# Performance work log

Hardware: AMD Instinct MI355X
Metric: run time of the kernel (lower is better)

The kernel has to match this reference:

```python
import jax, jax.numpy as jnp
from jax import lax
import numpy as np

P1, P2, M1, M2, WIN, STEP = 7, 7, 18, 55, 37, 4


def _unfold(x, p):
    # x: [N,C,Hp,Wp] -> [N, C*p*p, Ho*Wo], torch.nn.functional.unfold ordering (C, di, dj)
    N, C, Hp, Wp = x.shape
    Ho, Wo = Hp - p + 1, Wp - p + 1
    cols = jnp.stack([x[:, :, i:i + Ho, j:j + Wo] for i in range(p) for j in range(p)], axis=2)
    return cols.reshape(N, C * p * p, Ho * Wo)


def _reflect_unfold(x, r, p):
    return _unfold(jnp.pad(x, ((0, 0), (0, 0), (r, r), (r, r)), mode='reflect'), p)


def _fold(X, p, oh, ow):
    # inverse of unfold (sum of overlapping patches), torch.nn.functional.fold
    N, n, L = X.shape
    Ho, Wo = oh - p + 1, ow - p + 1
    C = n // (p * p)
    Xr = X.reshape(N, C, p, p, Ho, Wo)
    out = jnp.zeros((N, C, oh, ow), X.dtype)
    for i in range(p):
        for j in range(p):
            out = out.at[:, :, i:i + Ho, j:j + Wo].add(Xr[:, :, i, j])
    return out


def _block_matching(x, m, p, w, s):
    # x: [N,1,H,W] -> flat patch indices [N, B*m] into the (H+w-1)x(W+w-1) unfold grid
    N, C, H, Wd = x.shape
    inc = w // 2
    xs = _reflect_unfold(x, p // 2 + inc, p).reshape(N, p * p, H + 2 * inc, Wd + 2 * inc)
    xc = xs[:, :, inc:inc + H:s, inc:inc + Wd:s]  # [N, p*p, Hs, Ws]
    Hs, Ws = xc.shape[2], xc.shape[3]
    offs = jnp.stack(jnp.meshgrid(jnp.arange(w), jnp.arange(w), indexing='ij'), axis=-1).reshape(-1, 2)
    def d_of(off):
        xo = lax.dynamic_slice(xs, (0, 0, off[0], off[1]), (N, p * p, H, Wd))[:, :, ::s, ::s]
        return jnp.sum((xo - xc) ** 2, axis=1)  # [N, Hs, Ws]
    dist = jnp.moveaxis(lax.map(d_of, offs), 0, 1)  # [N, w*w, Hs, Ws]
    dist = dist.at[:, inc * w + inc].set(-1.0)  # force self-match first
    _, idx = lax.top_k(-jnp.transpose(dist, (0, 2, 3, 1)), m)  # smallest m, sorted
    idx = jnp.transpose(idx, (0, 3, 1, 2))  # [N, m, Hs, Ws]
    ir = idx // w - inc
    ic = idx % w - inc
    rows = inc + s * jnp.arange(Hs)
    cols = inc + s * jnp.arange(Ws)
    flat = (ir + rows[None, None, :, None]) * (Wd + w - 1) + (ic + cols[None, None, None, :])
    return jnp.transpose(flat.reshape(N, m, Hs * Ws), (0, 2, 1)).reshape(N, -1)  # [N, B*m]


def _group_patches(unf, idx, m, n):
    # unf: [N, n, L], idx: [N, B*m] -> [N, B, m, n]
    N = unf.shape[0]
    g = jnp.take_along_axis(unf, idx[:, None, :], axis=2)  # [N, n, B*m]
    return jnp.transpose(g, (0, 2, 1)).reshape(N, -1, m, n)


def _denoise1(Y, sigma):
    m, n = Y.shape[2], Y.shape[3]
    YtY = jnp.einsum('abik,abjk->abij', Y, Y)
    rhs = YtY - (n * sigma ** 2) * jnp.eye(m, dtype=Y.dtype)
    theta = jnp.swapaxes(jnp.linalg.solve(YtY, rhs), -1, -2)
    Xh = theta @ Y
    wts = 1.0 / jnp.sum(theta ** 2, axis=3, keepdims=True)
    return Xh, wts


def _denoise2(Y, X, sigma):
    m, n = X.shape[2], X.shape[3]
    XtX = jnp.einsum('abik,abjk->abij', X, X)
    A = XtX + (n * sigma ** 2) * jnp.eye(m, dtype=X.dtype)
    theta = jnp.swapaxes(jnp.linalg.solve(A, XtX), -1, -2)
    Xh = theta @ Y
    wts = 1.0 / jnp.sum(theta ** 2, axis=3, keepdims=True)
    return Xh, wts


def _aggregation(Y, wts, idx, H, Wd, L, p, w):
    # Y: [N,B,m,n], wts: [N,B,m,1], idx: [N,B*m]; scatter-add into unfold grid, fold, normalize
    N, B, m, n = Y.shape
    Yw = jnp.transpose(Y * wts, (0, 3, 1, 2)).reshape(N, n, B * m)
    wflat = jnp.broadcast_to(wts.reshape(N, 1, B * m), (N, n, B * m))
    def scat(vals, ib):
        return jnp.zeros((n, L), vals.dtype).at[:, ib].add(vals)
    Xsum = jax.vmap(scat)(Yw, idx)
    div = jax.vmap(scat)(wflat, idx)
    oh, ow = H + w - 1 + p - 1, Wd + w - 1 + p - 1
    num = _fold(Xsum, p, oh, ow)
    den = _fold(div, p, oh, ow)
    r = w // 2 + p // 2
    return (num / den)[:, :, r:-r, r:-r]


def _nlridge(input_y, sigma):
    N, C, H, Wd = input_y.shape
    w, s = WIN, STEP
    # ---- step 1 ----
    p, m = P1, M1
    yb = jnp.mean(input_y, axis=1, keepdims=True)
    idx1 = _block_matching(lax.stop_gradient(yb), m, p, w, s)
    unf_y1 = _reflect_unfold(input_y, p // 2 + w // 2, p)
    Y1 = _group_patches(unf_y1, idx1, m, C * p * p)
    Xh1, w1 = _denoise1(Y1, sigma)
    den1 = _aggregation(Xh1, w1, idx1, H, Wd, unf_y1.shape[2], p, w)
    # ---- step 2 ----
    p, m = P2, M2
    xb = jnp.mean(den1, axis=1, keepdims=True)
    idx2 = _block_matching(lax.stop_gradient(xb), m, p, w, s)
    unf_y2 = _reflect_unfold(input_y, p // 2 + w // 2, p)
    unf_x2 = _reflect_unfold(den1, p // 2 + w // 2, p)
    Y2 = _group_patches(unf_y2, idx2, m, C * p * p)
    X2 = _group_patches(unf_x2, idx2, m, C * p * p)
    Xh2, w2 = _denoise2(Y2, X2, sigma)
    return _aggregation(Xh2, w2, idx2, H, Wd, unf_y2.shape[2], p, w)


def setup_inputs() -> dict:
    key = jax.random.key(0)
    k1 = jax.random.fold_in(key, 1)
    input_y = jax.random.uniform(k1, (1, 1, 256, 256), dtype=jnp.float32)
    sigma = jnp.asarray(0.1, dtype=jnp.float32)  # ~25/255 AWGN
    return {"input_y": input_y, "sigma": sigma}


def reference(input_y, sigma):
    return _nlridge(input_y, sigma)
```

## Files before the change

### kernel.cpp

```cpp
#include <hip/hip_runtime.h>
#include <math.h>
#include <float.h>

constexpr int IMG  = 256;
constexpr int PADR = 21;
constexpr int PDIM = IMG + 2*PADR;
constexpr int XDIM = PDIM - 7 + 1;
constexpr int LTOT = XDIM * XDIM;
constexpr int WSZ  = 37;
constexpr int INC  = 18;
constexpr int ST   = 4;
constexpr int GDIM = 64;
constexpr int NBLK = GDIM * GDIM;
constexpr int PS   = 7;
constexpr int PP   = 49;
constexpr int MM1  = 18;
constexpr int MM2  = 55;
constexpr int RG   = 43;
constexpr int NOFF = WSZ * WSZ;
constexpr int UCAP = (NOFF + 63) / 64;
constexpr int TDIM = 43;
constexpr int TSZ  = TDIM * TDIM;
constexpr int SLABSTRIDE = 2 * TSZ;

__global__ void pad_reflect(const float* __restrict__ src, float* __restrict__ dst)
{
    int idx = blockIdx.x * 256 + threadIdx.x;
    if (idx >= PDIM * PDIM) return;
    int y = idx / PDIM, x = idx % PDIM;
    int oy = y - PADR; oy = (oy < 0) ? -oy : ((oy >= IMG) ? 2*(IMG-1) - oy : oy);
    int ox = x - PADR; ox = (ox < 0) ? -ox : ((ox >= IMG) ? 2*(IMG-1) - ox : ox);
    dst[idx] = src[oy * IMG + ox];
}

__global__ __launch_bounds__(256) void block_match(const float* __restrict__ pad,
                                                   int* __restrict__ pos, int m)
{
    __shared__ float reg[RG][RG + 1];
    __shared__ float dist[NOFF];

    const int gi = blockIdx.y, gj = blockIdx.x;
    const int tid = threadIdx.x;
    const int r0 = ST * gi, c0 = ST * gj;

    for (int t = tid; t < RG * RG; t += 256) {
        int r = t / RG, c = t % RG;
        reg[r][c] = pad[(r0 + r) * PDIM + (c0 + c)];
    }
    __syncthreads();

    float q[PP];
#pragma unroll
    for (int i = 0; i < PS; i++)
#pragma unroll
        for (int j = 0; j < PS; j++)
            q[i * PS + j] = reg[INC + i][INC + j];

    for (int o = tid; o < NOFF; o += 256) {
        int oi = o / WSZ, oj = o % WSZ;
        float s = 0.f;
#pragma unroll
        for (int i = 0; i < PS; i++)
#pragma unroll
            for (int j = 0; j < PS; j++) {
                float d = reg[oi + i][oj + j] - q[i * PS + j];
                s += d * d;
            }
        dist[o] = (o == INC * WSZ + INC) ? -1.0f : s;
    }
    __syncthreads();

    if (tid >= 64) return;
    const int lane = tid;

    float dv[UCAP];
#pragma unroll
    for (int u = 0; u < UCAP; u++) {
        int o = lane + (u << 6);
        dv[u] = (o < NOFF) ? dist[o] : FLT_MAX;
    }

    const int blk = gi * GDIM + gj;
    for (int sel = 0; sel < m; sel++) {
        float bv = dv[0]; int bo = lane;
#pragma unroll
        for (int u = 1; u < UCAP; u++) {
            int o = lane + (u << 6);
            if (dv[u] < bv) { bv = dv[u]; bo = o; }
        }
#pragma unroll
        for (int d = 1; d < 64; d <<= 1) {
            float ov = __shfl_xor(bv, d);
            int   oo = __shfl_xor(bo, d);
            if (ov < bv || (ov == bv && oo < bo)) { bv = ov; bo = oo; }
        }
        if (lane == 0) {
            int oi = bo / WSZ, oj = bo % WSZ;
            pos[blk * m + sel] = (oi + ST * gi) * XDIM + (oj + ST * gj);
        }
#pragma unroll
        for (int u = 0; u < UCAP; u++)
            if (bo == lane + (u << 6)) dv[u] = FLT_MAX;
    }
}

template<int M_, bool ADDC, bool SLAB>
__global__ __launch_bounds__(256) void denoise_scatter(
    const float* __restrict__ padY, const float* __restrict__ padS,
    const int* __restrict__ pos, const float* __restrict__ sigma_p,
    float* __restrict__ dst, float* __restrict__ Wacc)
{
    constexpr int MP = (M_ + 4) & ~3;
    constexpr int SS = 52;
    constexpr int YS = 60;
    constexpr int UN = (2 * TSZ > M_ * SS) ? 2 * TSZ : M_ * SS;

    __shared__ __align__(16) float Yt [PP * YS];
    __shared__ __align__(16) float Msh[M_ * MP];
    __shared__ __align__(16) float SorT[UN];
    __shared__ float pcol[M_];
    __shared__ float wsh[M_];
    __shared__ int   posh[M_];

    float* Ssh  = SorT;
    float* tile = SorT;

    const int tid = threadIdx.x;
    const int blk = blockIdx.x;
    const float sg = *sigma_p;
    const float c  = (float)PP * sg * sg;

    if (tid < M_) posh[tid] = pos[blk * M_ + tid];
    __syncthreads();

    for (int t = tid; t < M_ * SS; t += 256) {
        int k = t / SS, qq = t - (t / SS) * SS;
        float v = 0.f;
        if (qq < PP) {
            int p_ = posh[k];
            int a = p_ / XDIM, b = p_ - (p_ / XDIM) * XDIM;
            v = padS[(a + qq / PS) * PDIM + (b + qq % PS)];
        }
        Ssh[t] = v;
    }
    __syncthreads();

    for (int t = tid; t < M_ * M_; t += 256) {
        int i = t / M_, j = t - (t / M_) * M_;
        if (j > i) continue;
        const float4* Si = (const float4*)&Ssh[i * SS];
        const float4* Sj = (const float4*)&Ssh[j * SS];
        float acc = 0.f;
#pragma unroll
        for (int cch = 0; cch < SS / 4; cch++) {
            float4 a4 = Si[cch], b4 = Sj[cch];
            acc += a4.x * b4.x + a4.y * b4.y + a4.z * b4.z + a4.w * b4.w;
        }
        if (ADDC && i == j) acc += c;
        Msh[i * MP + j] = acc;
    }
    __syncthreads();

    if (tid < 64) {
        const int j = (tid < M_) ? tid : (M_ - 1);
        float col[M_];
#pragma unroll
        for (int i = 0; i < M_; i++)
            col[i] = Msh[(i >= j) ? (i * MP + j) : (j * MP + i)];

#pragma unroll 1
        for (int k = 0; k < M_; k++) {
            if (tid == k) {
#pragma unroll
                for (int i = 0; i < M_; i++) pcol[i] = col[i];
            }
            float piv = pcol[j];
            float d   = pcol[k];
            d = (fabsf(d) > 1e-30f) ? d : 1e-30f;
            float dinv = 1.0f / d;
            bool  isk  = (j == k);
            float f    = isk ? (1.0f - dinv) : (piv * dinv);
            float fix  = isk ? (-dinv)       : (piv * dinv);
            float negf = -f;
#pragma unroll
            for (int i = 0; i < M_; i++) {
                float b   = __int_as_float(
                    __builtin_amdgcn_readlane(__float_as_int(col[i]), k));
                float upd = fmaf(b, negf, col[i]);
                col[i] = (i == k) ? fix : upd;
            }
        }
        if (tid < M_) {
            float s = 0.f;
#pragma unroll
            for (int i = 0; i < M_; i++) {
                float th = fmaf(c, col[i], (i == j) ? 1.f : 0.f);
                s = fmaf(th, th, s);
            }
            wsh[j] = 1.0f / s;
#pragma unroll
            for (int i = 0; i < M_; i++)
                Msh[i * MP + j] = -col[i];
        } else if (tid < MP) {
#pragma unroll
            for (int i = 0; i < M_; i++)
                Msh[i * MP + tid] = 0.f;
        }
    } else {
        const int t0 = tid - 64;
        for (int t = t0; t < PP * MP; t += 192) {
            int qq = t / MP, k = t - (t / MP) * MP;
            float v = 0.f;
            if (k < M_) {
                int p_ = posh[k];
                int a = p_ / XDIM, b = p_ - (p_ / XDIM) * XDIM;
                v = padY[(a + qq / PS) * PDIM + (b + qq % PS)];
            }
            Yt[qq * YS + k] = v;
        }
        if (SLAB)
            for (int t = t0; t < 2 * TSZ; t += 192) tile[t] = 0.f;
    }
    __syncthreads();

    constexpr int KP = (M_ + 1) / 2;
    constexpr int QP = (PP + 1) / 2;
    const int r0 = ST * (blk >> 6), c0 = ST * (blk & (GDIM - 1));
    for (int t = tid; t < KP * QP; t += 256) {
        int kp = t / QP, qp = t - (t / QP) * QP;
        int k0 = kp * 2, k1 = k0 + 1;
        int qq0 = qp * 2, qq1 = qq0 + 1;
        bool k1v = (k1 < M_), q1v = (qq1 < PP);
        int k1c  = k1v ? k1 : k0;
        int qq1c = q1v ? qq1 : qq0;
        const float4* G0 = (const float4*)&Msh[k0  * MP];
        const float4* G1 = (const float4*)&Msh[k1c * MP];
        const float4* Y0 = (const float4*)&Yt [qq0  * YS];
        const float4* Y1 = (const float4*)&Yt [qq1c * YS];
        float z00 = 0.f, z01 = 0.f, z10 = 0.f, z11 = 0.f;
#pragma unroll
        for (int cch = 0; cch < MP / 4; cch++) {
            float4 g0 = G0[cch], g1 = G1[cch], y0 = Y0[cch], y1 = Y1[cch];
            z00 += g0.x*y0.x + g0.y*y0.y + g0.z*y0.z + g0.w*y0.w;
            z01 += g0.x*y1.x + g0.y*y1.y + g0.z*y1.z + g0.w*y1.w;
            z10 += g1.x*y0.x + g1.y*y0.y + g1.z*y0.z + g1.w*y0.w;
            z11 += g1.x*y1.x + g1.y*y1.y + g1.z*y1.z + g1.w*y1.w;
        }
        float w0 = wsh[k0], w1 = k1v ? wsh[k1] : 0.f;
        int p0 = posh[k0], p1 = posh[k1c];
        float xh00 = (Yt[qq0  * YS + k0 ] - c * z00) * w0;
        float xh01 = (Yt[qq1c * YS + k0 ] - c * z01) * w0;
        float xh10 = (Yt[qq0  * YS + k1c] - c * z10) * w1;
        float xh11 = (Yt[qq1c * YS + k1c] - c * z11) * w1;
        int a0 = p0 / XDIM, b0 = p0 - (p0 / XDIM) * XDIM;
        int a1 = p1 / XDIM, b1 = p1 - (p1 / XDIM) * XDIM;
        int i0 = qq0 / PS, j0 = qq0 - i0 * PS;
        int i1 = qq1 / PS, j1 = qq1 - i1 * PS;
        if (SLAB) {
            int u0 = a0 - r0, v0 = b0 - c0, u1 = a1 - r0, v1 = b1 - c0;
            int l00 = (u0 + i0) * TDIM + v0 + j0;
            int l10 = (u1 + i0) * TDIM + v1 + j0;
            atomicAdd(&tile[l00], xh00); atomicAdd(&tile[TSZ + l00], w0);
            atomicAdd(&tile[l10], xh10); atomicAdd(&tile[TSZ + l10], w1);
            if (q1v) {
                int l01 = (u0 + i1) * TDIM + v0 + j1;
                int l11 = (u1 + i1) * TDIM + v1 + j1;
                atomicAdd(&tile[l01], xh01); atomicAdd(&tile[TSZ + l01], w0);
                atomicAdd(&tile[l11], xh11); atomicAdd(&tile[TSZ + l11], w1);
            }
        } else {
            atomicAdd(&dst[qq0 * LTOT + p0], xh00);
            if (q1v) atomicAdd(&dst[qq1 * LTOT + p0], xh01);
            if (k1v) {
                atomicAdd(&dst[qq0 * LTOT + p1], xh10);
                if (q1v) atomicAdd(&dst[qq1 * LTOT + p1], xh11);
            }
        }
    }
    if (SLAB) {
        __syncthreads();
        float* g = dst + (size_t)blk * SLABSTRIDE;
        for (int t = tid; t < 2 * TSZ; t += 256) g[t] = tile[t];
    } else {
        for (int t = tid; t < M_; t += 256)
            atomicAdd(&Wacc[posh[t]], wsh[t]);
    }
}

__global__ void fold_slab(const float* __restrict__ slab, float* __restrict__ out)
{
    int idx = blockIdx.x * 256 + threadIdx.x;
    if (idx >= IMG * IMG) return;
    int y = (idx >> 8) + PADR, x = (idx & 255) + PADR;
    int qy = y >> 2, ry = y & 3;
    int qx = x >> 2, rx = x & 3;
    float num = 0.f, den = 0.f;
    for (int di = 0; di < 11; di++) {
        int gi = qy - di;
        int li = 4 * di + ry;
        if ((unsigned)gi > (unsigned)(GDIM - 1) || li >= TDIM) continue;
        for (int dj = 0; dj < 11; dj++) {
            int gj = qx - dj;
            int lj = 4 * dj + rx;
            if ((unsigned)gj > (unsigned)(GDIM - 1) || lj >= TDIM) continue;
            const float* s = slab + (size_t)((gi << 6) + gj) * SLABSTRIDE + li * TDIM + lj;
            num += s[0];
            den += s[TSZ];
        }
    }
    out[idx] = num / den;
}

__global__ void fold_norm(const float* __restrict__ Xsum, const float* __restrict__ Wacc,
                          float* __restrict__ out)
{
    int idx = blockIdx.x * 256 + threadIdx.x;
    if (idx >= IMG * IMG) return;
    int y0 = idx / IMG, x0 = idx % IMG;
    int y = y0 + PADR, x = x0 + PADR;
    float num = 0.f, den = 0.f;
#pragma unroll
    for (int i = 0; i < PS; i++)
#pragma unroll
        for (int j = 0; j < PS; j++) {
            int a = y - i, b = x - j;
            num += Xsum[(i * PS + j) * LTOT + a * XDIM + b];
            den += Wacc[a * XDIM + b];
        }
    out[idx] = num / den;
}

extern "C" void kernel_launch(void* const* d_in, const int* in_sizes, int n_in,
                              void* d_out, int out_size, void* d_ws, size_t ws_size,
                              hipStream_t stream)
{
    const float* input = (const float*)d_in[0];
    const float* sigma = (const float*)d_in[1];
    float* out = (float*)d_out;

    char* ws = (char*)d_ws;
    float* padY = (float*)ws; ws += (size_t)PDIM * PDIM * 4;
    float* padX = (float*)ws; ws += (size_t)PDIM * PDIM * 4;
    float* den1 = (float*)ws; ws += (size_t)IMG * IMG * 4;
    int*   pos  = (int*)ws;   ws += (size_t)NBLK * MM2 * 4;
    size_t head = (size_t)(ws - (char*)d_ws);
    size_t slabBytes = (size_t)NBLK * SLABSTRIDE * 4;

    const int padBlocks = (PDIM * PDIM + 255) / 256;
    const int imgBlocks = (IMG * IMG + 255) / 256;

    if (ws_size >= head + slabBytes) {
        float* slab = (float*)ws;

        pad_reflect<<<padBlocks, 256, 0, stream>>>(input, padY);
        block_match<<<dim3(GDIM, GDIM), 256, 0, stream>>>(padY, pos, MM1);
        denoise_scatter<MM1, false, true><<<NBLK, 256, 0, stream>>>(padY, padY, pos, sigma,
                                                                    slab, nullptr);
        fold_slab<<<imgBlocks, 256, 0, stream>>>(slab, den1);

        pad_reflect<<<padBlocks, 256, 0, stream>>>(den1, padX);
        block_match<<<dim3(GDIM, GDIM), 256, 0, stream>>>(padX, pos, MM2);
        denoise_scatter<MM2, true, true><<<NBLK, 256, 0, stream>>>(padY, padX, pos, sigma,
                                                                   slab, nullptr);
        fold_slab<<<imgBlocks, 256, 0, stream>>>(slab, out);
    } else {
        float* Xsum = (float*)ws; ws += (size_t)PP * LTOT * 4;
        float* Wacc = (float*)ws;

        hipMemsetAsync(Xsum, 0, (size_t)PP * LTOT * 4, stream);
        hipMemsetAsync(Wacc, 0, (size_t)LTOT * 4, stream);
        pad_reflect<<<padBlocks, 256, 0, stream>>>(input, padY);
        block_match<<<dim3(GDIM, GDIM), 256, 0, stream>>>(padY, pos, MM1);
        denoise_scatter<MM1, false, false><<<NBLK, 256, 0, stream>>>(padY, padY, pos, sigma,
                                                                     Xsum, Wacc);
        fold_norm<<<imgBlocks, 256, 0, stream>>>(Xsum, Wacc, den1);

        pad_reflect<<<padBlocks, 256, 0, stream>>>(den1, padX);
        hipMemsetAsync(Xsum, 0, (size_t)PP * LTOT * 4, stream);
        hipMemsetAsync(Wacc, 0, (size_t)LTOT * 4, stream);
        block_match<<<dim3(GDIM, GDIM), 256, 0, stream>>>(padX, pos, MM2);
        denoise_scatter<MM2, true, false><<<NBLK, 256, 0, stream>>>(padY, padX, pos, sigma,
                                                                    Xsum, Wacc);
        fold_norm<<<imgBlocks, 256, 0, stream>>>(Xsum, Wacc, out);
    }
}
```

Measured before the change: 1.096 ms.

## Accumulate denoised patches directly into global slab to shrink LDS and raise occupancy

Removes the per-block shared-memory tile and performs the patch/weight atomic adds straight into the block's global slab, which is now zeroed with a memset before each step. Ssh and Yt share one LDS buffer, the Gram loop only enumerates lower-triangle entries via a sqrt index map, launch bounds request more waves per SIMD, and the k/q pairing changes from adjacent to half-split. This is meant to cut LDS footprint and raise occupancy. In exchange it trades fast LDS atomics for global atomics and adds two large memsets.

```diff
diff --git a/kernel.cpp b/kernel.cpp
--- a/kernel.cpp
+++ b/kernel.cpp
@@ -105,25 +105,25 @@
 }
 
 template<int M_, bool ADDC, bool SLAB>
-__global__ __launch_bounds__(256) void denoise_scatter(
+__global__ __launch_bounds__(256, 5) void denoise_scatter(
     const float* __restrict__ padY, const float* __restrict__ padS,
     const int* __restrict__ pos, const float* __restrict__ sigma_p,
     float* __restrict__ dst, float* __restrict__ Wacc)
 {
-    constexpr int MP = (M_ + 4) & ~3;
-    constexpr int SS = 52;
-    constexpr int YS = 60;
-    constexpr int UN = (2 * TSZ > M_ * SS) ? 2 * TSZ : M_ * SS;
-
-    __shared__ __align__(16) float Yt [PP * YS];
+    constexpr int MP  = (M_ + 4) & ~3;
+    constexpr int SS  = 52;
+    constexpr int YS  = 60;
+    constexpr int TRI = M_ * (M_ + 1) / 2;
+    constexpr int UNF = (M_ * SS > PP * YS) ? M_ * SS : PP * YS;
+
+    __shared__ __align__(16) float SY [UNF];
     __shared__ __align__(16) float Msh[M_ * MP];
-    __shared__ __align__(16) float SorT[UN];
     __shared__ float pcol[M_];
     __shared__ float wsh[M_];
     __shared__ int   posh[M_];
 
-    float* Ssh  = SorT;
-    float* tile = SorT;
+    float* Ssh = SY;
+    float* Yt  = SY;
 
     const int tid = threadIdx.x;
     const int blk = blockIdx.x;
@@ -145,9 +145,11 @@
     }
     __syncthreads();
 
-    for (int t = tid; t < M_ * M_; t += 256) {
-        int i = t / M_, j = t - (t / M_) * M_;
-        if (j > i) continue;
+    for (int t = tid; t < TRI; t += 256) {
+        int i = (int)((sqrtf((float)(8 * t + 1)) - 1.f) * 0.5f);
+        if ((i + 1) * (i + 2) / 2 <= t) i++;
+        else if (i * (i + 1) / 2 > t) i--;
+        int j = t - i * (i + 1) / 2;
         const float4* Si = (const float4*)&Ssh[i * SS];
         const float4* Sj = (const float4*)&Ssh[j * SS];
         float acc = 0.f;
@@ -218,18 +220,17 @@
             }
             Yt[qq * YS + k] = v;
         }
-        if (SLAB)
-            for (int t = t0; t < 2 * TSZ; t += 192) tile[t] = 0.f;
     }
     __syncthreads();
 
     constexpr int KP = (M_ + 1) / 2;
     constexpr int QP = (PP + 1) / 2;
     const int r0 = ST * (blk >> 6), c0 = ST * (blk & (GDIM - 1));
+    float* slab = SLAB ? (dst + (size_t)blk * SLABSTRIDE) : dst;
     for (int t = tid; t < KP * QP; t += 256) {
         int kp = t / QP, qp = t - (t / QP) * QP;
-        int k0 = kp * 2, k1 = k0 + 1;
-        int qq0 = qp * 2, qq1 = qq0 + 1;
+        int k0 = kp,  k1 = kp + KP;
+        int qq0 = qp, qq1 = qp + QP;
         bool k1v = (k1 < M_), q1v = (qq1 < PP);
         int k1c  = k1v ? k1 : k0;
         int qq1c = q1v ? qq1 : qq0;
@@ -254,34 +255,30 @@
         float xh11 = (Yt[qq1c * YS + k1c] - c * z11) * w1;
         int a0 = p0 / XDIM, b0 = p0 - (p0 / XDIM) * XDIM;
         int a1 = p1 / XDIM, b1 = p1 - (p1 / XDIM) * XDIM;
-        int i0 = qq0 / PS, j0 = qq0 - i0 * PS;
-        int i1 = qq1 / PS, j1 = qq1 - i1 * PS;
+        int i0 = qq0 / PS,  j0 = qq0 - i0 * PS;
+        int i1 = qq1c / PS, j1 = qq1c - i1 * PS;
         if (SLAB) {
             int u0 = a0 - r0, v0 = b0 - c0, u1 = a1 - r0, v1 = b1 - c0;
             int l00 = (u0 + i0) * TDIM + v0 + j0;
             int l10 = (u1 + i0) * TDIM + v1 + j0;
-            atomicAdd(&tile[l00], xh00); atomicAdd(&tile[TSZ + l00], w0);
-            atomicAdd(&tile[l10], xh10); atomicAdd(&tile[TSZ + l10], w1);
+            atomicAdd(&slab[l00], xh00); atomicAdd(&slab[TSZ + l00], w0);
+            if (k1v) { atomicAdd(&slab[l10], xh10); atomicAdd(&slab[TSZ + l10], w1); }
             if (q1v) {
                 int l01 = (u0 + i1) * TDIM + v0 + j1;
                 int l11 = (u1 + i1) * TDIM + v1 + j1;
-                atomicAdd(&tile[l01], xh01); atomicAdd(&tile[TSZ + l01], w0);
-                atomicAdd(&tile[l11], xh11); atomicAdd(&tile[TSZ + l11], w1);
+                atomicAdd(&slab[l01], xh01); atomicAdd(&slab[TSZ + l01], w0);
+                if (k1v) { atomicAdd(&slab[l11], xh11); atomicAdd(&slab[TSZ + l11], w1); }
             }
         } else {
-            atomicAdd(&dst[qq0 * LTOT + p0], xh00);
-            if (q1v) atomicAdd(&dst[qq1 * LTOT + p0], xh01);
+            atomicAdd(&slab[qq0 * LTOT + p0], xh00);
+            if (q1v) atomicAdd(&slab[qq1 * LTOT + p0], xh01);
             if (k1v) {
-                atomicAdd(&dst[qq0 * LTOT + p1], xh10);
-                if (q1v) atomicAdd(&dst[qq1 * LTOT + p1], xh11);
-            }
-        }
-    }
-    if (SLAB) {
-        __syncthreads();
-        float* g = dst + (size_t)blk * SLABSTRIDE;
-        for (int t = tid; t < 2 * TSZ; t += 256) g[t] = tile[t];
-    } else {
+                atomicAdd(&slab[qq0 * LTOT + p1], xh10);
+                if (q1v) atomicAdd(&slab[qq1 * LTOT + p1], xh11);
+            }
+        }
+    }
+    if (!SLAB) {
         for (int t = tid; t < M_; t += 256)
             atomicAdd(&Wacc[posh[t]], wsh[t]);
     }
@@ -352,12 +349,14 @@
     if (ws_size >= head + slabBytes) {
         float* slab = (float*)ws;
 
+        hipMemsetAsync(slab, 0, slabBytes, stream);
         pad_reflect<<<padBlocks, 256, 0, stream>>>(input, padY);
         block_match<<<dim3(GDIM, GDIM), 256, 0, stream>>>(padY, pos, MM1);
         denoise_scatter<MM1, false, true><<<NBLK, 256, 0, stream>>>(padY, padY, pos, sigma,
                                                                     slab, nullptr);
         fold_slab<<<imgBlocks, 256, 0, stream>>>(slab, den1);
 
+        hipMemsetAsync(slab, 0, slabBytes, stream);
         pad_reflect<<<padBlocks, 256, 0, stream>>>(den1, padX);
         block_match<<<dim3(GDIM, GDIM), 256, 0, stream>>>(padX, pos, MM2);
         denoise_scatter<MM2, true, true><<<NBLK, 256, 0, stream>>>(padY, padX, pos, sigma,
```

Result: slower. 1.577 ms (+43.9%).
